# Optimization experiments

Measured on AMD Instinct MI355X. Metric: run time of the kernel, lower is better.

The kernel has to match this reference:

```python
import jax, jax.numpy as jnp
import numpy as np

B, N, V, D = 4, 1024, 20000, 512
DEPTH, H, DH, W = 6, 8, 64, 512
NB = N // W
NS = 512               # num_state_vectors
PM = D // 4            # dynamic pos-bias MLP width
XL_LAYERS = (4, 5)     # 0-indexed (config layers 5, 6)
REC_LAYER = 3          # 0-indexed (config layer 4)
QK_RMS = {3, 4, 5}     # recurrent + xl layers use qk rmsnorm
QK_SCALE = 8.0
FF = 4 * D


def _ln(x, g, eps=1e-5):
    mu = x.mean(-1, keepdims=True)
    var = ((x - mu) ** 2).mean(-1, keepdims=True)
    return (x - mu) * jax.lax.rsqrt(var + eps) * g


def _l2norm(x):
    return x * jax.lax.rsqrt((x * x).sum(-1, keepdims=True) + 1e-12)


def _pos_bias(pos_w1, pos_b1, pos_w2, pos_b2, pos_w3, pos_b3):
    # MLP over scalar relative distance -> per-head bias table [W, H]
    d = jnp.arange(W, dtype=jnp.float32)[:, None]
    h = jax.nn.silu(d @ pos_w1 + pos_b1)
    h = jax.nn.silu(h @ pos_w2 + pos_b2)
    table = h @ pos_w3 + pos_b3                       # [W, H]
    i = jnp.arange(W)[:, None]
    j = jnp.arange(2 * W)[None, :]
    rel = jnp.abs(i + W - j)                          # distance to key in [prev|cur] window
    win = (j > i) & (j <= i + W)                      # causal sliding window of width W
    pb = table[jnp.where(win, rel, 0)]                # [W, 2W, H]
    return jnp.transpose(pb, (2, 0, 1)), win          # [H, W, 2W], [W, 2W]


def setup_inputs() -> dict:
    key = jax.random.key(0)
    ks = iter(jax.random.split(key, 64))
    w = lambda shape, s=0.02: jax.random.normal(next(ks), shape, jnp.float32) * s
    return dict(
        x=jax.random.randint(next(ks), (B, N), 0, V, jnp.int32),
        tok_emb=w((V, D)),
        pos_w1=w((1, PM)), pos_b1=jnp.zeros((PM,), jnp.float32),
        pos_w2=w((PM, PM)), pos_b2=jnp.zeros((PM,), jnp.float32),
        pos_w3=w((PM, H)), pos_b3=jnp.zeros((H,), jnp.float32),
        ln_g=jnp.ones((DEPTH, D), jnp.float32),
        Wq=w((DEPTH, D, H * DH)), Wk=w((DEPTH, D, H * DH)),
        Wv=w((DEPTH, D, H * DH)), Wo=w((DEPTH, H * DH, D)),
        q_scale=jnp.ones((DEPTH, DH), jnp.float32),
        k_scale=jnp.ones((DEPTH, DH), jnp.float32),
        Wo_state=w((H * DH, D)),
        state_norm_g=jnp.ones((D,), jnp.float32),
        Wq2s=w((D, H * DH)), Ws2q=w((D, H * DH)), Ws2kv=w((D, 2 * DH)),
        W_state_out=w((H * DH, D)),
        ema_beta=jnp.zeros((D,), jnp.float32),
        ff_g=jnp.ones((DEPTH, D), jnp.float32),
        ff_w1=w((DEPTH, D, FF)), ff_b1=jnp.zeros((DEPTH, FF), jnp.float32),
        ff_w2=w((DEPTH, FF, D)), ff_b2=jnp.zeros((DEPTH, D), jnp.float32),
        final_g=jnp.ones((D,), jnp.float32),
        W_logits=w((D, V)),
        xl_mem_k=jax.random.normal(next(ks), (len(XL_LAYERS), B, W, H, DH), jnp.float32),
        xl_mem_v=jax.random.normal(next(ks), (len(XL_LAYERS), B, W, H, DH), jnp.float32),
        states=jax.random.normal(next(ks), (B, NS, D), jnp.float32),
    )


def reference(x, tok_emb, pos_w1, pos_b1, pos_w2, pos_b2, pos_w3, pos_b3,
              ln_g, Wq, Wk, Wv, Wo, q_scale, k_scale, Wo_state,
              state_norm_g, Wq2s, Ws2q, Ws2kv, W_state_out, ema_beta,
              ff_g, ff_w1, ff_b1, ff_w2, ff_b2, final_g, W_logits,
              xl_mem_k, xl_mem_v, states):
    pb, win = _pos_bias(pos_w1, pos_b1, pos_w2, pos_b2, pos_w3, pos_b3)
    j = jnp.arange(2 * W)
    no_mem = win & (j[None, :] >= W)                  # first block of a non-xl layer has no memory
    scale_dh = DH ** -0.5
    # enhanced recurrence: rotate the xl memory stack one layer down
    xk = jnp.roll(xl_mem_k, -1, axis=0)
    xv = jnp.roll(xl_mem_v, -1, axis=0)

    hstate = tok_emb[x]                               # [B, N, D]
    next_xl_k, next_xl_v = [], []
    next_states = states
    xl_idx = 0
    for l in range(DEPTH):
        xn = _ln(hstate, ln_g[l])
        q = (xn @ Wq[l]).reshape(B, N, H, DH)
        k = (xn @ Wk[l]).reshape(B, N, H, DH)
        v = (xn @ Wv[l]).reshape(B, N, H, DH)
        if l in QK_RMS:
            q = _l2norm(q) * q_scale[l]
            k = _l2norm(k) * k_scale[l]
            scale = QK_SCALE
        else:
            scale = scale_dh
        qb = q.reshape(B, NB, W, H, DH)
        kb = k.reshape(B, NB, W, H, DH)
        vb = v.reshape(B, NB, W, H, DH)
        is_xl = l in XL_LAYERS
        if is_xl:
            mem_k, mem_v = xk[xl_idx], xv[xl_idx]     # [B, W, H, DH] kv carried from prior call
            valid = jnp.stack([win] * NB)             # [NB, W, 2W]
        else:
            mem_k = jnp.zeros_like(kb[:, 0])
            mem_v = jnp.zeros_like(vb[:, 0])
            valid = jnp.stack([no_mem] + [win] * (NB - 1))
        # each block attends to [previous block | current block]
        pk = jnp.concatenate([mem_k[:, None], kb[:, :-1]], axis=1)
        pv = jnp.concatenate([mem_v[:, None], vb[:, :-1]], axis=1)
        kcat = jnp.concatenate([pk, kb], axis=2)      # [B, NB, 2W, H, DH]
        vcat = jnp.concatenate([pv, vb], axis=2)
        scores = jnp.einsum('bnihd,bnjhd->bnhij', qb * scale, kcat) + pb[None, None]
        scores = jnp.where(valid[None, :, None], scores, -1e9)
        attn = jax.nn.softmax(scores, axis=-1)
        out = jnp.einsum('bnhij,bnjhd->bnihd', attn, vcat).reshape(B, N, H * DH)
        branch = out @ Wo[l]
        if l == REC_LAYER:
            # recurrent state vectors: scan over blocks carrying states
            xn_blk = jnp.moveaxis(xn.reshape(B, NB, W, D), 1, 0)   # [NB, B, W, D]
            kb_s = jnp.moveaxis(kb, 1, 0)
            vb_s = jnp.moveaxis(vb, 1, 0)

            def step(st, inp):
                xb, kblk, vblk = inp
                sn = _ln(st, state_norm_g)
                s_k, s_v = jnp.split(sn @ Ws2kv, 2, axis=-1)       # single-head kv [B, NS, DH]
                # block tokens cross-attend to states
                q2s = (xb @ Wq2s).reshape(B, W, H, DH) * scale_dh
                a = jax.nn.softmax(jnp.einsum('bihd,bjd->bhij', q2s, s_k), -1)
                t_out = jnp.einsum('bhij,bjd->bihd', a, s_v).reshape(B, W, H * DH)
                # states attend to [states | block tokens]
                sq = (sn @ Ws2q).reshape(B, NS, H, DH) * scale_dh
                kc = jnp.concatenate([jnp.broadcast_to(s_k[:, :, None], (B, NS, H, DH)), kblk], axis=1)
                vc = jnp.concatenate([jnp.broadcast_to(s_v[:, :, None], (B, NS, H, DH)), vblk], axis=1)
                a2 = jax.nn.softmax(jnp.einsum('bihd,bjhd->bhij', sq, kc), -1)
                s_out = jnp.einsum('bhij,bjhd->bihd', a2, vc).reshape(B, NS, H * DH) @ W_state_out
                decay = jax.nn.sigmoid(ema_beta)
                return decay * st + (1.0 - decay) * s_out, t_out

            next_states, t_outs = jax.lax.scan(step, states, (xn_blk, kb_s, vb_s))
            to_state = jnp.moveaxis(t_outs, 0, 1).reshape(B, N, H * DH)
            branch = branch + to_state @ Wo_state
        hstate = hstate + branch
        if is_xl:
            next_xl_k.append(kb[:, -1])
            next_xl_v.append(vb[:, -1])
            xl_idx += 1
        fn = _ln(hstate, ff_g[l])
        hstate = hstate + (jax.nn.gelu(fn @ ff_w1[l] + ff_b1[l]) @ ff_w2[l] + ff_b2[l])

    logits = _ln(hstate, final_g) @ W_logits          # [B, N, V]
    return logits, jnp.stack(next_xl_k), jnp.stack(next_xl_v), next_states
```

## Files before the change

### kernel.cpp

```cpp
#include <hip/hip_runtime.h>
#include <math.h>


typedef __attribute__((ext_vector_type(8))) __bf16 bf16x8;
typedef __attribute__((ext_vector_type(8))) _Float16 f16x8;
typedef __attribute__((ext_vector_type(4))) float f32x4;

__device__ __forceinline__ ushort f2b(float f){
  uint u = __float_as_uint(f);
  uint r = (u + 0x7FFFu + ((u >> 16) & 1u)) >> 16;
  return (ushort)r;
}
__device__ __forceinline__ ushort f2h(float f){
  _Float16 h = (_Float16)f;
  return *reinterpret_cast<ushort*>(&h);
}
__device__ __forceinline__ uint pkh2(float a, float b){
  return (uint)f2h(a) | ((uint)f2h(b)<<16);
}

template<int MODE>
__global__ __launch_bounds__(256)
void k_prep(const float* __restrict__ src, ushort* __restrict__ dh,
            ushort* __restrict__ dl, int K, int N, int Npad, long zStride){
// ... 69 lines not shown
  ushort tmp[16];
#pragma unroll
  for (int u=0;u<16;u++) tmp[u] = tile[kf+u][d];
  uint4 o0 = make_uint4((uint)tmp[0]|((uint)tmp[1]<<16), (uint)tmp[2]|((uint)tmp[3]<<16),
                        (uint)tmp[4]|((uint)tmp[5]<<16), (uint)tmp[6]|((uint)tmp[7]<<16));
  uint4 o1 = make_uint4((uint)tmp[8]|((uint)tmp[9]<<16), (uint)tmp[10]|((uint)tmp[11]<<16),
                        (uint)tmp[12]|((uint)tmp[13]<<16),(uint)tmp[14]|((uint)tmp[15]<<16));
  *reinterpret_cast<uint4*>(dp)   = o0;
  *reinterpret_cast<uint4*>(dp+8) = o1;
}

__global__ void k_cvt(ushort* __restrict__ dst, const float* __restrict__ src, int n2){
  int idx = blockIdx.x*blockDim.x + threadIdx.x;
  if (idx >= n2) return;
  reinterpret_cast<uint*>(dst)[idx] = pkh2(src[2*idx], src[2*idx+1]);
}

__global__ void k_embed(const int* __restrict__ x, const float* __restrict__ emb,
                        float* __restrict__ h, int total4){
  int idx = blockIdx.x*blockDim.x + threadIdx.x;
  if (idx >= total4) return;
  int row = idx >> 7;
  int c4  = idx & 127;
  int tok = x[row];
  reinterpret_cast<float4*>(h)[idx] =
      reinterpret_cast<const float4*>(emb)[(size_t)tok*128 + c4];
}

__global__ void k_postable(const float* __restrict__ w1, const float* __restrict__ b1,
                           const float* __restrict__ w2, const float* __restrict__ b2,
                           const float* __restrict__ w3, const float* __restrict__ b3,
                           float* __restrict__ table){
  __shared__ float h1[128];
  __shared__ float h2[128];
  int d = blockIdx.x, t = threadIdx.x;
  float a = (float)d * w1[t] + b1[t];
  h1[t] = a / (1.f + __expf(-a));
  __syncthreads();
  float acc = b2[t];
  for (int p=0;p<128;p++) acc += h1[p]*w2[p*128+t];
  h2[t] = acc / (1.f + __expf(-acc));
  __syncthreads();
  if (t < 8){
    float acc2 = b3[t];
    for (int p=0;p<128;p++) acc2 += h2[p]*w3[p*8+t];
    table[d*8+t] = acc2;
  }
}

__global__ void k_ln(const float* __restrict__ x, const float* __restrict__ g,
                     ushort* __restrict__ y16,
                     ushort* __restrict__ yh, ushort* __restrict__ yl){
  int row = blockIdx.x;
  int t = threadIdx.x;
  float2 v = reinterpret_cast<const float2*>(x + (size_t)row*512)[t];
  float s = v.x+v.y, ss = v.x*v.x+v.y*v.y;
  for (int o=32;o;o>>=1){ s += __shfl_down(s,o); ss += __shfl_down(ss,o); }
  __shared__ float ls[4], lss[4];
  __shared__ float smu, srs;
  int wid = t>>6;
  if ((t&63)==0){ ls[wid]=s; lss[wid]=ss; }
  __syncthreads();
  if (t==0){
    float S=ls[0]+ls[1]+ls[2]+ls[3], SS=lss[0]+lss[1]+lss[2]+lss[3];
    float mu = S*(1.f/512.f);
    float var = SS*(1.f/512.f) - mu*mu;
    smu = mu; srs = rsqrtf(var + 1e-5f);
  }
  __syncthreads();
  float mu=smu, rs=srs;
  float2 gg = reinterpret_cast<const float2*>(g)[t];
  float ya = (v.x-mu)*rs*gg.x, yb = (v.y-mu)*rs*gg.y;
  size_t o2 = (size_t)row*512 + 2*t;
  if (y16)
    *reinterpret_cast<uint*>(&y16[o2]) = pkh2(ya, yb);
  if (yh){
    ushort ha = f2b(ya), hb = f2b(yb);
    *reinterpret_cast<uint*>(&yh[o2]) = (uint)ha | ((uint)hb<<16);
    float fa = __uint_as_float((uint)ha<<16), fb = __uint_as_float((uint)hb<<16);
    *reinterpret_cast<uint*>(&yl[o2]) = (uint)f2b(ya-fa) | ((uint)f2b(yb-fb)<<16);
  }
}

__global__ void k_qkrms16(float* __restrict__ q, float* __restrict__ k,
                          ushort* __restrict__ q16, ushort* __restrict__ k16,
                          const float* __restrict__ qs, const float* __restrict__ ks){
  int row = blockIdx.x;
  int h = threadIdx.x >> 6, d = threadIdx.x & 63;
  size_t base = (size_t)row*512 + h*64 + d;
  float qv = q[base];
  float s = qv*qv;
  for (int o=32;o;o>>=1) s += __shfl_xor(s,o);
  float qn = qv*rsqrtf(s+1e-12f)*qs[d];
  q[base] = qn; q16[base] = f2h(qn);
  float kv = k[base];
  float s2 = kv*kv;
  for (int o=32;o;o>>=1) s2 += __shfl_xor(s2,o);
  float kn = kv*rsqrtf(s2+1e-12f)*ks[d];
  k[base] = kn; k16[base] = f2h(kn);
}

__device__ __forceinline__ float geluf(float x){
  float u = 1.5957691216f*(x + 0.044715f*x*x*x);
  return x / (1.f + __expf(-u));
}

template<int ACC, int EPI, int OUT16>
__global__ __launch_bounds__(256)
void k_gemmh(const ushort* __restrict__ A, const ushort* __restrict__ Bt,
             const float* __restrict__ bias, float* __restrict__ C,
             ushort* __restrict__ C16, int M, int N, int K){
  __shared__ ushort As[128][68];
  __shared__ ushort Bs[128][68];
  const int t = threadIdx.x;
  const int m0 = blockIdx.x*128, n0 = blockIdx.y*128;
  const int w = t>>6, lane = t&63;
  const int wm = (w>>1)*64, wn = (w&1)*64;
  const int fr = lane&15, fg = lane>>4;
  const int srow = t>>1, sko = (t&1)*32;

  f32x4 acc[4][4];
#pragma unroll
  for (int i=0;i<4;i++)
#pragma unroll
    for (int j=0;j<4;j++){ acc[i][j][0]=0.f; acc[i][j][1]=0.f; acc[i][j][2]=0.f; acc[i][j][3]=0.f; }

  const ushort* ap = A  + (size_t)(m0+srow)*K + sko;
  const ushort* bp = Bt + (size_t)(n0+srow)*K + sko;

  for (int k0=0; k0<K; k0+=64){
    uint4 av[4], bv[4];
#pragma unroll
    for (int u=0;u<4;u++){
      av[u] = *reinterpret_cast<const uint4*>(ap + k0 + u*8);
      bv[u] = *reinterpret_cast<const uint4*>(bp + k0 + u*8);
    }
#pragma unroll
    for (int u=0;u<4;u++){
      *reinterpret_cast<uint4*>(&As[srow][sko+u*8]) = av[u];
      *reinterpret_cast<uint4*>(&Bs[srow][sko+u*8]) = bv[u];
    }
    __syncthreads();
#pragma unroll
    for (int kk=0;kk<2;kk++){
      f16x8 af[4], bf[4];
#pragma unroll
      for (int mi=0;mi<4;mi++)
        af[mi] = *reinterpret_cast<const f16x8*>(&As[wm+mi*16+fr][kk*32+fg*8]);
#pragma unroll
      for (int nj=0;nj<4;nj++)
        bf[nj] = *reinterpret_cast<const f16x8*>(&Bs[wn+nj*16+fr][kk*32+fg*8]);
#pragma unroll
      for (int mi=0;mi<4;mi++)
#pragma unroll
        for (int nj=0;nj<4;nj++)
          acc[mi][nj] = __builtin_amdgcn_mfma_f32_16x16x32_f16(af[mi], bf[nj], acc[mi][nj], 0,0,0);
    }
    __syncthreads();
  }
#pragma unroll
  for (int mi=0;mi<4;mi++){
#pragma unroll
    for (int r=0;r<4;r++){
      int row = m0 + wm + mi*16 + fg*4 + r;
#pragma unroll
      for (int nj=0;nj<4;nj++){
        int col = n0 + wn + nj*16 + fr;
        if (col < N){
          float val = acc[mi][nj][r];
          if (bias) val += bias[col];
          if (EPI==1) val = geluf(val);
          if (OUT16){
            C16[(size_t)row*N + col] = f2h(val);
          } else {
            if (ACC) C[(size_t)row*N + col] += val; else C[(size_t)row*N + col] = val;
          }
        }
      }
    }
  }
}

template<int ACC, int EPI, int OUT16, int VT>
__global__ __launch_bounds__(256)
void k_gemmh64(const ushort* __restrict__ A, const ushort* __restrict__ Bt,
               const float* __restrict__ bias, float* __restrict__ C,
               ushort* __restrict__ C16, ushort* __restrict__ vT,
               int M, int N, int K){
  __shared__ ushort As[64][68];
  __shared__ ushort Bs[128][68];
  const int t = threadIdx.x;
  const int m0 = blockIdx.x*64, n0 = blockIdx.y*128;
  const int w = t>>6, lane = t&63;
  const int wm = (w>>1)*32, wn = (w&1)*64;
  const int fr = lane&15, fg = lane>>4;
  const int srowA = t>>2, skoA = (t&3)*16;
  const int srowB = t>>1, skoB = (t&1)*32;

  f32x4 acc[2][4];
#pragma unroll
  for (int i=0;i<2;i++)
#pragma unroll
    for (int j=0;j<4;j++){ acc[i][j][0]=0.f; acc[i][j][1]=0.f; acc[i][j][2]=0.f; acc[i][j][3]=0.f; }

  const ushort* ap = A  + (size_t)(m0+srowA)*K + skoA;
  const ushort* bp = Bt + (size_t)(n0+srowB)*K + skoB;

  for (int k0=0; k0<K; k0+=64){
    uint4 a0 = *reinterpret_cast<const uint4*>(ap + k0);
    uint4 a1 = *reinterpret_cast<const uint4*>(ap + k0 + 8);
    uint4 b0 = *reinterpret_cast<const uint4*>(bp + k0);
    uint4 b1 = *reinterpret_cast<const uint4*>(bp + k0 + 8);
    uint4 b2 = *reinterpret_cast<const uint4*>(bp + k0 + 16);
    uint4 b3 = *reinterpret_cast<const uint4*>(bp + k0 + 24);
    *reinterpret_cast<uint4*>(&As[srowA][skoA])    = a0;
    *reinterpret_cast<uint4*>(&As[srowA][skoA+8])  = a1;
    *reinterpret_cast<uint4*>(&Bs[srowB][skoB])    = b0;
    *reinterpret_cast<uint4*>(&Bs[srowB][skoB+8])  = b1;
    *reinterpret_cast<uint4*>(&Bs[srowB][skoB+16]) = b2;
    *reinterpret_cast<uint4*>(&Bs[srowB][skoB+24]) = b3;
    __syncthreads();
#pragma unroll
    for (int kk=0;kk<2;kk++){
      f16x8 af[2], bf[4];
#pragma unroll
      for (int mi=0;mi<2;mi++)
        af[mi] = *reinterpret_cast<const f16x8*>(&As[wm+mi*16+fr][kk*32+fg*8]);
#pragma unroll
      for (int nj=0;nj<4;nj++)
        bf[nj] = *reinterpret_cast<const f16x8*>(&Bs[wn+nj*16+fr][kk*32+fg*8]);
#pragma unroll
      for (int mi=0;mi<2;mi++)
#pragma unroll
        for (int nj=0;nj<4;nj++)
          acc[mi][nj] = __builtin_amdgcn_mfma_f32_16x16x32_f16(af[mi], bf[nj], acc[mi][nj], 0,0,0);
    }
    __syncthreads();
  }
#pragma unroll
  for (int mi=0;mi<2;mi++){
#pragma unroll
    for (int r=0;r<4;r++){
      int row = m0 + wm + mi*16 + fg*4 + r;
#pragma unroll
      for (int nj=0;nj<4;nj++){
        int col = n0 + wn + nj*16 + fr;
        if (col < N){
          float val = acc[mi][nj][r];
          if (EPI==2){
            size_t idx = (size_t)row*N + col;
            float old = C[idx];
            float dec = 1.f/(1.f+__expf(-bias[col]));
            C[idx] = dec*old + (1.f-dec)*val;
          } else {
            if (bias) val += bias[col];
            if (EPI==1) val = geluf(val);
            if (OUT16){
              C16[(size_t)row*N + col] = f2h(val);
            } else {
              if (ACC) C[(size_t)row*N + col] += val; else C[(size_t)row*N + col] = val;
            }
          }
        }
      }
    }
  }
  if (VT){
#pragma unroll
    for (int mi=0;mi<2;mi++)
#pragma unroll
      for (int r=0;r<4;r++)
#pragma unroll
        for (int nj=0;nj<4;nj++)
          Bs[wn+nj*16+fr][wm+mi*16+fg*4+r] = f2h(acc[mi][nj][r]);
    __syncthreads();
    int c = t>>1, half = t&1;
    int hh = (n0+c)>>6, dd = (n0+c)&63;
    int bb = m0>>10, posb = m0&1023;
    ushort* dp = vT + (size_t)bb*524288 + (size_t)hh*65536 + (size_t)dd*1024 + posb + half*32;
#pragma unroll
    for (int u=0;u<4;u++)
      *reinterpret_cast<uint4*>(dp + u*8) = *reinterpret_cast<const uint4*>(&Bs[c][half*32 + u*8]);
  }
}

template<int REMAP>
__global__ __launch_bounds__(256)
void k_gemm_sp(const ushort* __restrict__ Ah, const ushort* __restrict__ Al,
               const ushort* __restrict__ Bh, const ushort* __restrict__ Bl,
               float* __restrict__ C1, ushort* __restrict__ C1h, int ld1, int N1,
               float* __restrict__ C2, ushort* __restrict__ C2h, int ld2,
               int nb, int M, int N, int K){
  __shared__ ushort As[2][128][36];
  __shared__ ushort Bs[2][128][36];
  const int t = threadIdx.x;
  const int m0 = blockIdx.x*128, n0 = blockIdx.y*128;
  const int w = t>>6, lane = t&63;
  const int wm = (w>>1)*64, wn = (w&1)*64;
  const int fr = lane&15, fg = lane>>4;
  const int srow = t>>1, sko = (t&1)*16;

  f32x4 acc[4][4];
#pragma unroll
  for (int i=0;i<4;i++)
#pragma unroll
    for (int j=0;j<4;j++){ acc[i][j][0]=0.f; acc[i][j][1]=0.f; acc[i][j][2]=0.f; acc[i][j][3]=0.f; }

  int mrow = m0 + srow;
  int arow = REMAP ? ((mrow>>9)*1024 + nb*512 + (mrow&511)) : mrow;
  const ushort* aph = Ah + (size_t)arow*K + sko;
  const ushort* apl = Al + (size_t)arow*K + sko;
  const ushort* bph = Bh + (size_t)(n0+srow)*K + sko;
  const ushort* bpl = Bl + (size_t)(n0+srow)*K + sko;

  for (int k0=0; k0<K; k0+=32){
    uint4 a0 = *reinterpret_cast<const uint4*>(aph + k0);
    uint4 a1 = *reinterpret_cast<const uint4*>(aph + k0 + 8);
    uint4 al0 = *reinterpret_cast<const uint4*>(apl + k0);
    uint4 al1 = *reinterpret_cast<const uint4*>(apl + k0 + 8);
    uint4 b0 = *reinterpret_cast<const uint4*>(bph + k0);
    uint4 b1 = *reinterpret_cast<const uint4*>(bph + k0 + 8);
    uint4 bl0 = *reinterpret_cast<const uint4*>(bpl + k0);
    uint4 bl1 = *reinterpret_cast<const uint4*>(bpl + k0 + 8);
    *reinterpret_cast<uint4*>(&As[0][srow][sko])   = a0;
    *reinterpret_cast<uint4*>(&As[0][srow][sko+8]) = a1;
    *reinterpret_cast<uint4*>(&As[1][srow][sko])   = al0;
    *reinterpret_cast<uint4*>(&As[1][srow][sko+8]) = al1;
    *reinterpret_cast<uint4*>(&Bs[0][srow][sko])   = b0;
    *reinterpret_cast<uint4*>(&Bs[0][srow][sko+8]) = b1;
    *reinterpret_cast<uint4*>(&Bs[1][srow][sko])   = bl0;
    *reinterpret_cast<uint4*>(&Bs[1][srow][sko+8]) = bl1;
    __syncthreads();

    bf16x8 ah[4], al[4], bh[4], bl[4];
#pragma unroll
    for (int mi=0;mi<4;mi++){
      ah[mi] = *reinterpret_cast<const bf16x8*>(&As[0][wm+mi*16+fr][fg*8]);
      al[mi] = *reinterpret_cast<const bf16x8*>(&As[1][wm+mi*16+fr][fg*8]);
    }
#pragma unroll
    for (int nj=0;nj<4;nj++){
      bh[nj] = *reinterpret_cast<const bf16x8*>(&Bs[0][wn+nj*16+fr][fg*8]);
      bl[nj] = *reinterpret_cast<const bf16x8*>(&Bs[1][wn+nj*16+fr][fg*8]);
    }
#pragma unroll
    for (int mi=0;mi<4;mi++)
#pragma unroll
      for (int nj=0;nj<4;nj++){
        acc[mi][nj] = __builtin_amdgcn_mfma_f32_16x16x32_bf16(ah[mi], bh[nj], acc[mi][nj], 0,0,0);
        acc[mi][nj] = __builtin_amdgcn_mfma_f32_16x16x32_bf16(al[mi], bh[nj], acc[mi][nj], 0,0,0);
        acc[mi][nj] = __builtin_amdgcn_mfma_f32_16x16x32_bf16(ah[mi], bl[nj], acc[mi][nj], 0,0,0);
      }
    __syncthreads();
  }
#pragma unroll
  for (int mi=0;mi<4;mi++){
#pragma unroll
    for (int r=0;r<4;r++){
      int row = m0 + wm + mi*16 + fg*4 + r;
#pragma unroll
      for (int nj=0;nj<4;nj++){
        int col = n0 + wn + nj*16 + fr;
        float val = acc[mi][nj][r];
        if (col < N1){
          if (C1)  C1[(size_t)row*ld1 + col] = val;
          if (C1h) C1h[(size_t)row*ld1 + col] = f2h(val);
        } else if (col < N){
          if (C2)  C2[(size_t)row*ld2 + (col-N1)] = val;
          if (C2h) C2h[(size_t)row*ld2 + (col-N1)] = f2h(val);
        }
      }
    }
  }
}

__global__ __launch_bounds__(256)
void k_attn_win(const ushort* __restrict__ q16, const ushort* __restrict__ k16,
                const ushort* __restrict__ vTb,
                const ushort* __restrict__ xlK, const ushort* __restrict__ xlVT,
                int isxl, ushort* __restrict__ O, float scale,
                const float* __restrict__ table){
  __shared__ ushort Qs[64][72];
  __shared__ ushort Ks[64][72];
  __shared__ ushort Vs[64][72];
  __shared__ ushort Pw[4][16][72];
  __shared__ float tcol[512];
  const int b = blockIdx.z, h = blockIdx.y;
  const int nb = blockIdx.x>>3, qt = blockIdx.x&7;
  const int t = threadIdx.x, w = t>>6, lane = t&63;
  const int fr = lane&15, fg = lane>>4;
  tcol[t]     = table[t*8 + h];
  tcol[t+256] = table[(t+256)*8 + h];

  const ushort* Q  = q16 + (size_t)nb*262144;
  const ushort* K1 = k16 + (size_t)nb*262144;
  const ushort* V1 = vTb + (size_t)nb*512;
  ushort* Op = O + (size_t)nb*262144;
  const int has_mem = (nb==1) || isxl;
  const ushort* K0; long k0B; const ushort* V0; long vt0B, vt0H; int vt0D;
  if (nb==1){ K0=k16; k0B=524288; V0=vTb; vt0B=524288; vt0H=65536; vt0D=1024; }
  else if (isxl){ K0=xlK; k0B=262144; V0=xlVT; vt0B=262144; vt0H=32768; vt0D=512; }
  else { K0=k16; k0B=524288; V0=vTb; vt0B=524288; vt0H=65536; vt0D=1024; }

  {
    int qrow = t>>2, doff = (t&3)*16;
    const ushort* qp = Q + (size_t)b*524288 + (size_t)(qt*64+qrow)*512 + h*64 + doff;
    *reinterpret_cast<uint4*>(&Qs[qrow][doff])   = *reinterpret_cast<const uint4*>(qp);
    *reinterpret_cast<uint4*>(&Qs[qrow][doff+8]) = *reinterpret_cast<const uint4*>(qp+8);
  }
  __syncthreads();
  f16x8 aq[2];
  aq[0] = *reinterpret_cast<const f16x8*>(&Qs[w*16+fr][fg*8]);
  aq[1] = *reinterpret_cast<const f16x8*>(&Qs[w*16+fr][32+fg*8]);

  f32x4 so[4];
#pragma unroll
  for (int dt=0;dt<4;dt++){ so[dt][0]=0.f; so[dt][1]=0.f; so[dt][2]=0.f; so[dt][3]=0.f; }
  float m[4] = {-1e30f,-1e30f,-1e30f,-1e30f};
  float lsum[4] = {0.f,0.f,0.f,0.f};

  const int srow = t>>2, sdo = (t&3)*16;
  const int vd = t>>2,   vkf = (t&3)*16;

  int jt0 = has_mem ? qt : 8;
  int jt1 = qt + 8; if (jt1 > 15) jt1 = 15;

  for (int jt=jt0; jt<=jt1; jt++){
    {
      int key = jt*64 + srow;
      const ushort* kp;
      if (key < 512) kp = K0 + (size_t)b*k0B + (size_t)key*512 + h*64 + sdo;
      else           kp = K1 + (size_t)b*524288 + (size_t)(key-512)*512 + h*64 + sdo;
      *reinterpret_cast<uint4*>(&Ks[srow][sdo])   = *reinterpret_cast<const uint4*>(kp);
      *reinterpret_cast<uint4*>(&Ks[srow][sdo+8]) = *reinterpret_cast<const uint4*>(kp+8);
    }
    {
      const ushort* vp;
      if (jt*64 < 512) vp = V0 + (size_t)b*vt0B + (size_t)h*vt0H + (size_t)vd*vt0D + jt*64 + vkf;
      else             vp = V1 + (size_t)b*524288 + (size_t)h*65536 + (size_t)vd*1024 + (jt*64-512) + vkf;
      *reinterpret_cast<uint4*>(&Vs[vd][vkf])   = *reinterpret_cast<const uint4*>(vp);
      *reinterpret_cast<uint4*>(&Vs[vd][vkf+8]) = *reinterpret_cast<const uint4*>(vp+8);
    }
    __syncthreads();
    f32x4 sacc[4];
#pragma unroll
    for (int kt=0;kt<4;kt++){ sacc[kt][0]=0.f; sacc[kt][1]=0.f; sacc[kt][2]=0.f; sacc[kt][3]=0.f; }
#pragma unroll
    for (int ks=0;ks<2;ks++){
#pragma unroll
      for (int kt=0;kt<4;kt++){
        f16x8 bf = *reinterpret_cast<const f16x8*>(&Ks[kt*16+fr][ks*32+fg*8]);
        sacc[kt] = __builtin_amdgcn_mfma_f32_16x16x32_f16(aq[ks], bf, sacc[kt], 0,0,0);
      }
    }
#pragma unroll
    for (int r=0;r<4;r++){
      float sv[4];
      int ia = qt*64 + w*16 + fg*4 + r;
#pragma unroll
      for (int kt=0;kt<4;kt++){
        float s = sacc[kt][r]*scale;
        int jg = jt*64 + kt*16 + fr;
        bool valid = (jg > ia) && (jg <= ia+512) && (has_mem || jg >= 512);
        sv[kt] = valid ? s + tcol[ia+512-jg] : -1e9f;
      }
      float tm = fmaxf(fmaxf(sv[0],sv[1]), fmaxf(sv[2],sv[3]));
      tm = fmaxf(tm, __shfl_xor(tm,1));
      tm = fmaxf(tm, __shfl_xor(tm,2));
      tm = fmaxf(tm, __shfl_xor(tm,4));
      tm = fmaxf(tm, __shfl_xor(tm,8));
      float mn = fmaxf(m[r], tm);
      float c = __expf(m[r]-mn);
      m[r] = mn;
      float ps = 0.f;
#pragma unroll
      for (int kt=0;kt<4;kt++){
        float pp = (sv[kt] <= -1e8f) ? 0.f : __expf(sv[kt]-mn);
        ps += pp;
        Pw[w][fg*4+r][kt*16+fr] = f2h(pp);
      }
      ps += __shfl_xor(ps,1);
      ps += __shfl_xor(ps,2);
      ps += __shfl_xor(ps,4);
      ps += __shfl_xor(ps,8);
      lsum[r] = lsum[r]*c + ps;
#pragma unroll
      for (int dt=0;dt<4;dt++) so[dt][r] *= c;
    }
#pragma unroll
    for (int ks=0;ks<2;ks++){
      f16x8 pa = *reinterpret_cast<const f16x8*>(&Pw[w][fr][ks*32+fg*8]);
#pragma unroll
      for (int dt=0;dt<4;dt++){
        f16x8 bv = *reinterpret_cast<const f16x8*>(&Vs[dt*16+fr][ks*32+fg*8]);
        so[dt] = __builtin_amdgcn_mfma_f32_16x16x32_f16(pa, bv, so[dt], 0,0,0);
      }
    }
    __syncthreads();
  }
#pragma unroll
  for (int r=0;r<4;r++){
    int row = qt*64 + w*16 + fg*4 + r;
    float inv = 1.f / lsum[r];
    ushort* op = Op + (size_t)b*524288 + (size_t)row*512 + h*64;
#pragma unroll
    for (int dt=0;dt<4;dt++)
      op[dt*16+fr] = f2h(so[dt][r]*inv);
  }
}

__global__ __launch_bounds__(256)
void k_attn_plain(const ushort* __restrict__ Q, long qB,
                  const ushort* __restrict__ K0, long k0B, int k0R, int k0H,
                  const ushort* __restrict__ K1, long k1B, int k1R, int k1H,
                  const ushort* __restrict__ VT0, long vt0B, long vt0H, int vt0D,
                  const ushort* __restrict__ VT1, long vt1B, long vt1H, int vt1D,
                  int n0, int n1,
                  ushort* __restrict__ O, long oB, float scale){
  __shared__ ushort Qs[64][72];
  __shared__ ushort Ks[64][72];
  __shared__ ushort Vs[64][72];
  __shared__ ushort Pw[4][16][72];
  const int b = blockIdx.z, h = blockIdx.y, qt = blockIdx.x;
  const int t = threadIdx.x, w = t>>6, lane = t&63;
  const int fr = lane&15, fg = lane>>4;
  {
    int qrow = t>>2, doff = (t&3)*16;
    const ushort* qp = Q + (size_t)b*qB + (size_t)(qt*64+qrow)*512 + h*64 + doff;
    *reinterpret_cast<uint4*>(&Qs[qrow][doff])   = *reinterpret_cast<const uint4*>(qp);
    *reinterpret_cast<uint4*>(&Qs[qrow][doff+8]) = *reinterpret_cast<const uint4*>(qp+8);
  }
  __syncthreads();
  f16x8 aq[2];
  aq[0] = *reinterpret_cast<const f16x8*>(&Qs[w*16+fr][fg*8]);
  aq[1] = *reinterpret_cast<const f16x8*>(&Qs[w*16+fr][32+fg*8]);

  f32x4 so[4];
#pragma unroll
  for (int dt=0;dt<4;dt++){ so[dt][0]=0.f; so[dt][1]=0.f; so[dt][2]=0.f; so[dt][3]=0.f; }
  float m[4] = {-1e30f,-1e30f,-1e30f,-1e30f};
  float lsum[4] = {0.f,0.f,0.f,0.f};

  const int nt = (n0+n1)>>6;
  const int srow = t>>2, sdo = (t&3)*16;
  const int vd = t>>2,   vkf = (t&3)*16;

  for (int jt=0; jt<nt; jt++){
    {
      int key = jt*64 + srow;
      const ushort* kp;
      if (key < n0) kp = K0 + (size_t)b*k0B + (size_t)key*k0R + (k0H? h*64:0) + sdo;
      else          kp = K1 + (size_t)b*k1B + (size_t)(key-n0)*k1R + (k1H? h*64:0) + sdo;
      *reinterpret_cast<uint4*>(&Ks[srow][sdo])   = *reinterpret_cast<const uint4*>(kp);
      *reinterpret_cast<uint4*>(&Ks[srow][sdo+8]) = *reinterpret_cast<const uint4*>(kp+8);
    }
    {
      const ushort* vp;
      if (jt*64 < n0) vp = VT0 + (size_t)b*vt0B + (size_t)h*vt0H + (size_t)vd*vt0D + jt*64 + vkf;
      else            vp = VT1 + (size_t)b*vt1B + (size_t)h*vt1H + (size_t)vd*vt1D + (jt*64-n0) + vkf;
      *reinterpret_cast<uint4*>(&Vs[vd][vkf])   = *reinterpret_cast<const uint4*>(vp);
      *reinterpret_cast<uint4*>(&Vs[vd][vkf+8]) = *reinterpret_cast<const uint4*>(vp+8);
    }
    __syncthreads();
    f32x4 sacc[4];
#pragma unroll
    for (int kt=0;kt<4;kt++){ sacc[kt][0]=0.f; sacc[kt][1]=0.f; sacc[kt][2]=0.f; sacc[kt][3]=0.f; }
#pragma unroll
    for (int ks=0;ks<2;ks++){
#pragma unroll
      for (int kt=0;kt<4;kt++){
        f16x8 bf = *reinterpret_cast<const f16x8*>(&Ks[kt*16+fr][ks*32+fg*8]);
        sacc[kt] = __builtin_amdgcn_mfma_f32_16x16x32_f16(aq[ks], bf, sacc[kt], 0,0,0);
      }
    }
#pragma unroll
    for (int r=0;r<4;r++){
      float sv[4];
#pragma unroll
      for (int kt=0;kt<4;kt++) sv[kt] = sacc[kt][r]*scale;
      float tm = fmaxf(fmaxf(sv[0],sv[1]), fmaxf(sv[2],sv[3]));
      tm = fmaxf(tm, __shfl_xor(tm,1));
      tm = fmaxf(tm, __shfl_xor(tm,2));
      tm = fmaxf(tm, __shfl_xor(tm,4));
      tm = fmaxf(tm, __shfl_xor(tm,8));
      float mn = fmaxf(m[r], tm);
      float c = __expf(m[r]-mn);
      m[r] = mn;
      float ps = 0.f;
#pragma unroll
      for (int kt=0;kt<4;kt++){
        float pp = __expf(sv[kt]-mn);
        ps += pp;
        Pw[w][fg*4+r][kt*16+fr] = f2h(pp);
      }
      ps += __shfl_xor(ps,1);
      ps += __shfl_xor(ps,2);
      ps += __shfl_xor(ps,4);
      ps += __shfl_xor(ps,8);
      lsum[r] = lsum[r]*c + ps;
#pragma unroll
      for (int dt=0;dt<4;dt++) so[dt][r] *= c;
    }
#pragma unroll
    for (int ks=0;ks<2;ks++){
      f16x8 pa = *reinterpret_cast<const f16x8*>(&Pw[w][fr][ks*32+fg*8]);
#pragma unroll
      for (int dt=0;dt<4;dt++){
        f16x8 bv = *reinterpret_cast<const f16x8*>(&Vs[dt*16+fr][ks*32+fg*8]);
        so[dt] = __builtin_amdgcn_mfma_f32_16x16x32_f16(pa, bv, so[dt], 0,0,0);
      }
    }
    __syncthreads();
  }
#pragma unroll
  for (int r=0;r<4;r++){
    int row = qt*64 + w*16 + fg*4 + r;
    float inv = 1.f / lsum[r];
    ushort* op = O + (size_t)b*oB + (size_t)row*512 + h*64;
#pragma unroll
    for (int dt=0;dt<4;dt++)
      op[dt*16+fr] = f2h(so[dt][r]*inv);
  }
}

__global__ void k_copy(float* __restrict__ dst, const float* __restrict__ src, int n){
  int idx = blockIdx.x*blockDim.x + threadIdx.x;
  if (idx < n) dst[idx] = src[idx];
}
__global__ void k_xlout(float* __restrict__ dk, float* __restrict__ dv,
                        const float* __restrict__ k, const float* __restrict__ v){
  int idx = blockIdx.x*blockDim.x + threadIdx.x;
  if (idx >= 1048576) return;
  int b = idx >> 18, rem = idx & 262143;
  size_t s = (size_t)b*524288 + 262144 + rem;
  dk[idx] = k[s]; dv[idx] = v[s];
}

extern "C" void kernel_launch(void* const* d_in, const int* in_sizes, int n_in,
                              void* d_out, int out_size, void* d_ws, size_t ws_size,
                              hipStream_t stream){
  if (ws_size < (size_t)160579584) return;

  const int*   x        = (const int*)  d_in[0];
  const float* tok_emb  = (const float*)d_in[1];
  const float* pw1 = (const float*)d_in[2];
  const float* pb1 = (const float*)d_in[3];
  const float* pw2 = (const float*)d_in[4];
  const float* pb2 = (const float*)d_in[5];
  const float* pw3 = (const float*)d_in[6];
  const float* pb3 = (const float*)d_in[7];
  const float* ln_g = (const float*)d_in[8];
  const float* Wq = (const float*)d_in[9];
  const float* Wk = (const float*)d_in[10];
  const float* Wv = (const float*)d_in[11];
  const float* Wo = (const float*)d_in[12];
  const float* q_scale = (const float*)d_in[13];
  const float* k_scale = (const float*)d_in[14];
  const float* Wo_state = (const float*)d_in[15];
  const float* state_norm_g = (const float*)d_in[16];
  const float* Wq2s = (const float*)d_in[17];
  const float* Ws2q = (const float*)d_in[18];
  const float* Ws2kv = (const float*)d_in[19];
  const float* W_state_out = (const float*)d_in[20];
  const float* ema_beta = (const float*)d_in[21];
  const float* ff_g = (const float*)d_in[22];
  const float* ff_w1 = (const float*)d_in[23];
  const float* ff_b1 = (const float*)d_in[24];
  const float* ff_w2 = (const float*)d_in[25];
  const float* ff_b2 = (const float*)d_in[26];
  const float* final_g = (const float*)d_in[27];
  const float* W_logits = (const float*)d_in[28];
  const float* xl_mem_k = (const float*)d_in[29];
  const float* xl_mem_v = (const float*)d_in[30];
  const float* states_in = (const float*)d_in[31];

  float* out = (float*)d_out;
  float* out_xlk    = out + 81920000;
  float* out_xlv    = out + 84017152;
  float* out_states = out + 86114304;

  float* p = (float*)d_ws;
  float* hstate   = p; p += 2097152;
  float* q        = p; p += 2097152;
  float* k        = p; p += 2097152;
  float* v        = p; p += 2097152;
  float* states_cur = p; p += 1048576;
  float* table    = p; p += 4096;

  ushort* us = (ushort*)p;
  ushort* wqkh  = us; us += 3145728;
  ushort* wqkl  = us; us += 3145728;
  ushort* wvT   = us; us += 1572864;
  ushort* woT   = us; us += 1572864;
  ushort* ffw1T = us; us += 6291456;
  ushort* ffw2T = us; us += 6291456;
  ushort* wostT = us; us += 262144;
  ushort* wstoutT = us; us += 262144;
  ushort* wq2sh = us; us += 262144;
  ushort* wq2sl = us; us += 262144;
  ushort* wsqkvh = us; us += 327680;
  ushort* wsqkvl = us; us += 327680;
  ushort* wlogT  = us; us += 10289152;
  ushort* vTb   = us; us += 2097152;
  ushort* xlvT  = us; us += 2097152;
  ushort* svT   = us; us += 131072;
  ushort* xn16  = us; us += 2097152;
  ushort* ao16  = us; us += 2097152;
  ushort* ff1_16 = us; us += 8388608;
  ushort* xnh   = us; us += 2097152;
  ushort* xnl   = us; us += 2097152;
  ushort* q16   = us; us += 2097152;
  ushort* k16   = us; us += 2097152;
  ushort* xlk16 = us; us += 2097152;
  ushort* ts16   = ff1_16;
  ushort* sa16   = ff1_16 + 2097152;
  ushort* snh    = ff1_16 + 3145728;
  ushort* snl    = ff1_16 + 4194304;
  ushort* sq16   = ff1_16 + 5242880;
  ushort* q2s16  = ff1_16 + 6291456;
  ushort* skv16  = ff1_16 + 7340032;

  k_prep<1><<<dim3(16,16,6),256,0,stream>>>(Wq, wqkh, wqkl, 512,512,512, 524288);
  k_prep<1><<<dim3(16,16,6),256,0,stream>>>(Wk, wqkh+262144, wqkl+262144, 512,512,512, 524288);
  k_prep<0><<<dim3(16,16,6),256,0,stream>>>(Wv, wvT, nullptr, 512,512,512, 262144);
  k_prep<0><<<dim3(16,16,6),256,0,stream>>>(Wo, woT, nullptr, 512,512,512, 262144);
  k_prep<0><<<dim3(64,16,6),256,0,stream>>>(ff_w1, ffw1T, nullptr, 512,2048,2048, 1048576);
  k_prep<0><<<dim3(16,64,6),256,0,stream>>>(ff_w2, ffw2T, nullptr, 2048,512,512, 1048576);
  k_prep<0><<<dim3(16,16,1),256,0,stream>>>(Wo_state, wostT, nullptr, 512,512,512, 262144);
  k_prep<0><<<dim3(16,16,1),256,0,stream>>>(W_state_out, wstoutT, nullptr, 512,512,512, 262144);
  k_prep<1><<<dim3(16,16,1),256,0,stream>>>(Wq2s, wq2sh, wq2sl, 512,512,512, 262144);
  k_prep<1><<<dim3(16,16,1),256,0,stream>>>(Ws2q, wsqkvh, wsqkvl, 512,512,512, 327680);
  k_prep<1><<<dim3(4,16,1),256,0,stream>>>(Ws2kv, wsqkvh+262144, wsqkvl+262144, 512,128,128, 327680);
  k_prep<0><<<dim3(628,16,1),256,0,stream>>>(W_logits, wlogT, nullptr, 512,20000,20096, 10289152);

  for (int s=0;s<2;s++)
    k_vtrans<<<dim3(8,8,4),256,0,stream>>>(xl_mem_v + (size_t)s*1048576,
                                           xlvT + (size_t)s*1048576,
                                           262144L, 512, 1, 262144L, 32768L, 512);
  k_cvt<<<4096,256,0,stream>>>(xlk16, xl_mem_k, 1048576);

  k_embed<<<2048, 256, 0, stream>>>(x, tok_emb, hstate, 524288);
  k_postable<<<512, 128, 0, stream>>>(pw1,pb1,pw2,pb2,pw3,pb3, table);
  k_copy<<<4096, 256, 0, stream>>>(states_cur, states_in, 1048576);

  for (int l=0;l<6;l++){
    k_ln<<<4096,256,0,stream>>>(hstate, ln_g + l*512, xn16, xnh, xnl);
    float scale = 0.125f;
    if (l>=3){
      k_gemm_sp<0><<<dim3(32,8),256,0,stream>>>(xnh, xnl,
          wqkh + (size_t)l*524288, wqkl + (size_t)l*524288,
          q, nullptr, 512, 512, k, nullptr, 512, 0, 4096, 1024, 512);
      k_qkrms16<<<4096,512,0,stream>>>(q, k, q16, k16, q_scale + l*64, k_scale + l*64);
      scale = 8.f;
    } else {
      k_gemm_sp<0><<<dim3(32,8),256,0,stream>>>(xnh, xnl,
          wqkh + (size_t)l*524288, wqkl + (size_t)l*524288,
          nullptr, q16, 512, 512, nullptr, k16, 512, 0, 4096, 1024, 512);
    }
    k_gemmh64<0,0,0,1><<<dim3(64,4),256,0,stream>>>(xn16, wvT + (size_t)l*262144, nullptr, v, nullptr, vTb, 4096,512,512);

    bool isxl = (l==4 || l==5);
    int src = (l==4)? 1 : 0;
    k_attn_win<<<dim3(16,8,4),256,0,stream>>>(
        q16, k16, vTb,
        isxl ? xlk16 + (size_t)src*1048576 : k16,
        isxl ? xlvT  + (size_t)src*1048576 : vTb,
        isxl ? 1 : 0, ao16, scale, table);

    k_gemmh64<1,0,0,0><<<dim3(64,4),256,0,stream>>>(ao16, woT + (size_t)l*262144, nullptr, hstate, nullptr, nullptr, 4096,512,512);
    if (l==3){
      for (int nb=0;nb<2;nb++){
        k_ln<<<2048,256,0,stream>>>(states_cur, state_norm_g, nullptr, snh, snl);
        k_gemm_sp<0><<<dim3(16,5),256,0,stream>>>(snh, snl, wsqkvh, wsqkvl,
            nullptr, sq16, 512, 512, nullptr, skv16, 128, 0, 2048, 640, 512);
        k_vtrans16<<<dim3(8,1,4),256,0,stream>>>(skv16 + 64, svT, 65536L, 128, 32768L, 512);
        k_gemm_sp<1><<<dim3(16,4),256,0,stream>>>(xnh, xnl, wq2sh, wq2sl,
            nullptr, q2s16, 512, 512, nullptr, nullptr, 0, nb, 2048, 512, 512);
        k_attn_plain<<<dim3(8,8,4),256,0,stream>>>(
          q2s16, 262144L,
          skv16, 65536L, 128, 0,
          skv16, 65536L, 128, 0,
          svT, 32768L, 0L, 512,
          svT, 32768L, 0L, 512,
          512, 0,
          ts16 + nb*262144, 524288L, 0.125f);
        k_attn_plain<<<dim3(8,8,4),256,0,stream>>>(
          sq16, 262144L,
          skv16, 65536L, 128, 0,
          k16 + nb*262144, 524288L, 512, 1,
          svT, 32768L, 0L, 512,
          vTb + nb*512, 524288L, 65536L, 1024,
          512, 512,
          sa16, 262144L, 0.125f);
        k_gemmh64<0,2,0,0><<<dim3(32,4),256,0,stream>>>(sa16, wstoutT, ema_beta, states_cur, nullptr, nullptr, 2048,512,512);
      }
      k_gemmh64<1,0,0,0><<<dim3(64,4),256,0,stream>>>(ts16, wostT, nullptr, hstate, nullptr, nullptr, 4096,512,512);
    }
    if (isxl){
      int xli = l-4;
      k_xlout<<<4096,256,0,stream>>>(out_xlk + (size_t)xli*1048576,
                                     out_xlv + (size_t)xli*1048576, k, v);
    }
    k_ln<<<4096,256,0,stream>>>(hstate, ff_g + l*512, xn16, nullptr, nullptr);
    k_gemmh<0,1,1><<<dim3(32,16),256,0,stream>>>(xn16, ffw1T + (size_t)l*1048576, ff_b1 + l*2048, nullptr, ff1_16, 4096,2048,512);
    k_gemmh64<1,0,0,0><<<dim3(64,4),256,0,stream>>>(ff1_16, ffw2T + (size_t)l*1048576, ff_b2 + l*512, hstate, nullptr, nullptr, 4096,512,2048);
  }
  k_ln<<<4096,256,0,stream>>>(hstate, final_g, xn16, nullptr, nullptr);
  k_gemmh<0,0,0><<<dim3(32,157),256,0,stream>>>(xn16, wlogT, nullptr, out, nullptr, 4096,20000,512);
  k_copy<<<4096, 256, 0, stream>>>(out_states, states_cur, 1048576);
}
```

Before: 1.728 ms.

## Fuse QK RMSnorm and XL cache output into GEMM epilogues, merge recurrent attention

Moves the per-head QK L2-normalisation into the QK projection GEMM epilogue, using lane shuffles to reduce across the 64-wide head tile. The XL key/value cache outputs are now written straight from the QK and V GEMM epilogues, so the fp32 q/k/v buffers and the separate normalisation and copy kernels are gone. The two recurrent-state attention launches are merged into one kernel that picks its task from blockIdx. This cuts launches and fp32 intermediate traffic, at the cost of more complex epilogues and a reliance on each wave's 64 columns lining up with a single head.

```diff
diff --git a/kernel.cpp b/kernel.cpp
--- a/kernel.cpp
+++ b/kernel.cpp
@@ -175,24 +175,6 @@
   }
 }
 
-__global__ void k_qkrms16(float* __restrict__ q, float* __restrict__ k,
-                          ushort* __restrict__ q16, ushort* __restrict__ k16,
-                          const float* __restrict__ qs, const float* __restrict__ ks){
-  int row = blockIdx.x;
-  int h = threadIdx.x >> 6, d = threadIdx.x & 63;
-  size_t base = (size_t)row*512 + h*64 + d;
-  float qv = q[base];
-  float s = qv*qv;
-  for (int o=32;o;o>>=1) s += __shfl_xor(s,o);
-  float qn = qv*rsqrtf(s+1e-12f)*qs[d];
-  q[base] = qn; q16[base] = f2h(qn);
-  float kv = k[base];
-  float s2 = kv*kv;
-  for (int o=32;o;o>>=1) s2 += __shfl_xor(s2,o);
-  float kn = kv*rsqrtf(s2+1e-12f)*ks[d];
-  k[base] = kn; k16[base] = f2h(kn);
-}
-
 __device__ __forceinline__ float geluf(float x){
   float u = 1.5957691216f*(x + 0.044715f*x*x*x);
   return x / (1.f + __expf(-u));
@@ -279,7 +261,7 @@
 void k_gemmh64(const ushort* __restrict__ A, const ushort* __restrict__ Bt,
                const float* __restrict__ bias, float* __restrict__ C,
                ushort* __restrict__ C16, ushort* __restrict__ vT,
-               int M, int N, int K){
+               float* __restrict__ xlv, int M, int N, int K){
   __shared__ ushort As[64][68];
   __shared__ ushort Bs[128][68];
   const int t = threadIdx.x;
@@ -349,10 +331,12 @@
             if (bias) val += bias[col];
             if (EPI==1) val = geluf(val);
             if (OUT16){
-              C16[(size_t)row*N + col] = f2h(val);
-            } else {
+              if (C16) C16[(size_t)row*N + col] = f2h(val);
+            } else if (C){
               if (ACC) C[(size_t)row*N + col] += val; else C[(size_t)row*N + col] = val;
             }
+            if (VT && xlv && (row&1023) >= 512)
+              xlv[((size_t)(row>>10)*512 + (row&1023) - 512)*512 + col] = val;
           }
         }
       }
@@ -381,8 +365,10 @@
 __global__ __launch_bounds__(256)
 void k_gemm_sp(const ushort* __restrict__ Ah, const ushort* __restrict__ Al,
                const ushort* __restrict__ Bh, const ushort* __restrict__ Bl,
-               float* __restrict__ C1, ushort* __restrict__ C1h, int ld1, int N1,
-               float* __restrict__ C2, ushort* __restrict__ C2h, int ld2,
+               ushort* __restrict__ C1h, int ld1, int N1,
+               ushort* __restrict__ C2h, int ld2,
+               const float* __restrict__ qsc, const float* __restrict__ ksc,
+               float* __restrict__ xlk,
                int nb, int M, int N, int K){
   __shared__ ushort As[2][128][36];
   __shared__ ushort Bs[2][128][36];
@@ -451,16 +437,30 @@
 #pragma unroll
     for (int r=0;r<4;r++){
       int row = m0 + wm + mi*16 + fg*4 + r;
+      float vals[4];
+#pragma unroll
+      for (int nj=0;nj<4;nj++) vals[nj] = acc[mi][nj][r];
+      if (qsc){
+        float ss = vals[0]*vals[0]+vals[1]*vals[1]+vals[2]*vals[2]+vals[3]*vals[3];
+        ss += __shfl_xor(ss,1);
+        ss += __shfl_xor(ss,2);
+        ss += __shfl_xor(ss,4);
+        ss += __shfl_xor(ss,8);
+        float rs = rsqrtf(ss + 1e-12f);
+        const float* sc = ((n0+wn) < N1) ? qsc : ksc;
+#pragma unroll
+        for (int nj=0;nj<4;nj++) vals[nj] = vals[nj]*rs*sc[nj*16+fr];
+      }
 #pragma unroll
       for (int nj=0;nj<4;nj++){
         int col = n0 + wn + nj*16 + fr;
-        float val = acc[mi][nj][r];
+        float val = vals[nj];
         if (col < N1){
-          if (C1)  C1[(size_t)row*ld1 + col] = val;
           if (C1h) C1h[(size_t)row*ld1 + col] = f2h(val);
         } else if (col < N){
-          if (C2)  C2[(size_t)row*ld2 + (col-N1)] = val;
           if (C2h) C2h[(size_t)row*ld2 + (col-N1)] = f2h(val);
+          if (xlk && (row&1023) >= 512)
+            xlk[((size_t)(row>>10)*512 + (row&1023) - 512)*512 + (col-N1)] = val;
         }
       }
     }
@@ -603,23 +603,35 @@
 }
 
 __global__ __launch_bounds__(256)
-void k_attn_plain(const ushort* __restrict__ Q, long qB,
-                  const ushort* __restrict__ K0, long k0B, int k0R, int k0H,
-                  const ushort* __restrict__ K1, long k1B, int k1R, int k1H,
-                  const ushort* __restrict__ VT0, long vt0B, long vt0H, int vt0D,
-                  const ushort* __restrict__ VT1, long vt1B, long vt1H, int vt1D,
-                  int n0, int n1,
-                  ushort* __restrict__ O, long oB, float scale){
+void k_attn_rec(const ushort* __restrict__ q2s, const ushort* __restrict__ sq,
+                const ushort* __restrict__ skv, const ushort* __restrict__ svT,
+                const ushort* __restrict__ kblk, const ushort* __restrict__ vblk,
+                ushort* __restrict__ ts, ushort* __restrict__ sa){
   __shared__ ushort Qs[64][72];
   __shared__ ushort Ks[64][72];
   __shared__ ushort Vs[64][72];
   __shared__ ushort Pw[4][16][72];
-  const int b = blockIdx.z, h = blockIdx.y, qt = blockIdx.x;
+  const int b = blockIdx.z, h = blockIdx.y;
+  const int task = blockIdx.x>>3, qt = blockIdx.x&7;
   const int t = threadIdx.x, w = t>>6, lane = t&63;
   const int fr = lane&15, fg = lane>>4;
+
+  const ushort* Q; const ushort* K1; int k1R, k1H;
+  const ushort* VT1; long vt1B, vt1H; int vt1D;
+  int nt; ushort* O; long oB;
+  if (task==0){
+    Q=q2s; K1=skv; k1R=128; k1H=0;
+    VT1=svT; vt1B=32768; vt1H=0; vt1D=512;
+    nt=8; O=ts; oB=524288;
+  } else {
+    Q=sq; K1=kblk; k1R=512; k1H=1;
+    VT1=vblk; vt1B=524288; vt1H=65536; vt1D=1024;
+    nt=16; O=sa; oB=262144;
+  }
+
   {
     int qrow = t>>2, doff = (t&3)*16;
-    const ushort* qp = Q + (size_t)b*qB + (size_t)(qt*64+qrow)*512 + h*64 + doff;
+    const ushort* qp = Q + (size_t)b*262144 + (size_t)(qt*64+qrow)*512 + h*64 + doff;
     *reinterpret_cast<uint4*>(&Qs[qrow][doff])   = *reinterpret_cast<const uint4*>(qp);
     *reinterpret_cast<uint4*>(&Qs[qrow][doff+8]) = *reinterpret_cast<const uint4*>(qp+8);
   }
@@ -634,7 +646,6 @@
   float m[4] = {-1e30f,-1e30f,-1e30f,-1e30f};
   float lsum[4] = {0.f,0.f,0.f,0.f};
 
-  const int nt = (n0+n1)>>6;
   const int srow = t>>2, sdo = (t&3)*16;
   const int vd = t>>2,   vkf = (t&3)*16;
 
@@ -642,15 +653,15 @@
     {
       int key = jt*64 + srow;
       const ushort* kp;
-      if (key < n0) kp = K0 + (size_t)b*k0B + (size_t)key*k0R + (k0H? h*64:0) + sdo;
-      else          kp = K1 + (size_t)b*k1B + (size_t)(key-n0)*k1R + (k1H? h*64:0) + sdo;
+      if (key < 512) kp = skv + (size_t)b*65536 + (size_t)key*128 + sdo;
+      else           kp = K1 + (size_t)b*524288 + (size_t)(key-512)*k1R + (k1H? h*64:0) + sdo;
       *reinterpret_cast<uint4*>(&Ks[srow][sdo])   = *reinterpret_cast<const uint4*>(kp);
       *reinterpret_cast<uint4*>(&Ks[srow][sdo+8]) = *reinterpret_cast<const uint4*>(kp+8);
     }
     {
       const ushort* vp;
-      if (jt*64 < n0) vp = VT0 + (size_t)b*vt0B + (size_t)h*vt0H + (size_t)vd*vt0D + jt*64 + vkf;
-      else            vp = VT1 + (size_t)b*vt1B + (size_t)h*vt1H + (size_t)vd*vt1D + (jt*64-n0) + vkf;
+      if (jt*64 < 512) vp = svT + (size_t)b*32768 + (size_t)vd*512 + jt*64 + vkf;
+      else             vp = VT1 + (size_t)b*vt1B + (size_t)h*vt1H + (size_t)vd*vt1D + (jt*64-512) + vkf;
       *reinterpret_cast<uint4*>(&Vs[vd][vkf])   = *reinterpret_cast<const uint4*>(vp);
       *reinterpret_cast<uint4*>(&Vs[vd][vkf+8]) = *reinterpret_cast<const uint4*>(vp+8);
     }
@@ -670,7 +681,7 @@
     for (int r=0;r<4;r++){
       float sv[4];
 #pragma unroll
-      for (int kt=0;kt<4;kt++) sv[kt] = sacc[kt][r]*scale;
+      for (int kt=0;kt<4;kt++) sv[kt] = sacc[kt][r]*0.125f;
       float tm = fmaxf(fmaxf(sv[0],sv[1]), fmaxf(sv[2],sv[3]));
       tm = fmaxf(tm, __shfl_xor(tm,1));
       tm = fmaxf(tm, __shfl_xor(tm,2));
@@ -720,19 +731,11 @@
   int idx = blockIdx.x*blockDim.x + threadIdx.x;
   if (idx < n) dst[idx] = src[idx];
 }
-__global__ void k_xlout(float* __restrict__ dk, float* __restrict__ dv,
-                        const float* __restrict__ k, const float* __restrict__ v){
-  int idx = blockIdx.x*blockDim.x + threadIdx.x;
-  if (idx >= 1048576) return;
-  int b = idx >> 18, rem = idx & 262143;
-  size_t s = (size_t)b*524288 + 262144 + rem;
-  dk[idx] = k[s]; dv[idx] = v[s];
-}
 
 extern "C" void kernel_launch(void* const* d_in, const int* in_sizes, int n_in,
                               void* d_out, int out_size, void* d_ws, size_t ws_size,
                               hipStream_t stream){
-  if (ws_size < (size_t)160579584) return;
+  if (ws_size < (size_t)135413760) return;
 
   const int*   x        = (const int*)  d_in[0];
   const float* tok_emb  = (const float*)d_in[1];
@@ -774,9 +777,6 @@
 
   float* p = (float*)d_ws;
   float* hstate   = p; p += 2097152;
-  float* q        = p; p += 2097152;
-  float* k        = p; p += 2097152;
-  float* v        = p; p += 2097152;
   float* states_cur = p; p += 1048576;
   float* table    = p; p += 4096;
 
@@ -837,66 +837,51 @@
   k_copy<<<4096, 256, 0, stream>>>(states_cur, states_in, 1048576);
 
   for (int l=0;l<6;l++){
+    bool isxl = (l==4 || l==5);
+    int xli = l-4;
+    int src = (l==4)? 1 : 0;
     k_ln<<<4096,256,0,stream>>>(hstate, ln_g + l*512, xn16, xnh, xnl);
     float scale = 0.125f;
-    if (l>=3){
-      k_gemm_sp<0><<<dim3(32,8),256,0,stream>>>(xnh, xnl,
-          wqkh + (size_t)l*524288, wqkl + (size_t)l*524288,
-          q, nullptr, 512, 512, k, nullptr, 512, 0, 4096, 1024, 512);
-      k_qkrms16<<<4096,512,0,stream>>>(q, k, q16, k16, q_scale + l*64, k_scale + l*64);
-      scale = 8.f;
-    } else {
-      k_gemm_sp<0><<<dim3(32,8),256,0,stream>>>(xnh, xnl,
-          wqkh + (size_t)l*524288, wqkl + (size_t)l*524288,
-          nullptr, q16, 512, 512, nullptr, k16, 512, 0, 4096, 1024, 512);
-    }
-    k_gemmh64<0,0,0,1><<<dim3(64,4),256,0,stream>>>(xn16, wvT + (size_t)l*262144, nullptr, v, nullptr, vTb, 4096,512,512);
-
-    bool isxl = (l==4 || l==5);
-    int src = (l==4)? 1 : 0;
+    const float* qsc = nullptr; const float* ksc = nullptr;
+    if (l>=3){ qsc = q_scale + l*64; ksc = k_scale + l*64; scale = 8.f; }
+    k_gemm_sp<0><<<dim3(32,8),256,0,stream>>>(xnh, xnl,
+        wqkh + (size_t)l*524288, wqkl + (size_t)l*524288,
+        q16, 512, 512, k16, 512, qsc, ksc,
+        isxl ? out_xlk + (size_t)xli*1048576 : nullptr,
+        0, 4096, 1024, 512);
+    k_gemmh64<0,0,0,1><<<dim3(64,4),256,0,stream>>>(xn16, wvT + (size_t)l*262144,
+        nullptr, nullptr, nullptr, vTb,
+        isxl ? out_xlv + (size_t)xli*1048576 : nullptr, 4096,512,512);
+
     k_attn_win<<<dim3(16,8,4),256,0,stream>>>(
         q16, k16, vTb,
         isxl ? xlk16 + (size_t)src*1048576 : k16,
         isxl ? xlvT  + (size_t)src*1048576 : vTb,
         isxl ? 1 : 0, ao16, scale, table);
 
-    k_gemmh64<1,0,0,0><<<dim3(64,4),256,0,stream>>>(ao16, woT + (size_t)l*262144, nullptr, hstate, nullptr, nullptr, 4096,512,512);
+    k_gemmh64<1,0,0,0><<<dim3(64,4),256,0,stream>>>(ao16, woT + (size_t)l*262144,
+        nullptr, hstate, nullptr, nullptr, nullptr, 4096,512,512);
     if (l==3){
       for (int nb=0;nb<2;nb++){
         k_ln<<<2048,256,0,stream>>>(states_cur, state_norm_g, nullptr, snh, snl);
         k_gemm_sp<0><<<dim3(16,5),256,0,stream>>>(snh, snl, wsqkvh, wsqkvl,
-            nullptr, sq16, 512, 512, nullptr, skv16, 128, 0, 2048, 640, 512);
+            sq16, 512, 512, skv16, 128, nullptr, nullptr, nullptr, 0, 2048, 640, 512);
         k_vtrans16<<<dim3(8,1,4),256,0,stream>>>(skv16 + 64, svT, 65536L, 128, 32768L, 512);
         k_gemm_sp<1><<<dim3(16,4),256,0,stream>>>(xnh, xnl, wq2sh, wq2sl,
-            nullptr, q2s16, 512, 512, nullptr, nullptr, 0, nb, 2048, 512, 512);
-        k_attn_plain<<<dim3(8,8,4),256,0,stream>>>(
-          q2s16, 262144L,
-          skv16, 65536L, 128, 0,
-          skv16, 65536L, 128, 0,
-          svT, 32768L, 0L, 512,
-          svT, 32768L, 0L, 512,
-          512, 0,
-          ts16 + nb*262144, 524288L, 0.125f);
-        k_attn_plain<<<dim3(8,8,4),256,0,stream>>>(
-          sq16, 262144L,
-          skv16, 65536L, 128, 0,
-          k16 + nb*262144, 524288L, 512, 1,
-          svT, 32768L, 0L, 512,
-          vTb + nb*512, 524288L, 65536L, 1024,
-          512, 512,
-          sa16, 262144L, 0.125f);
-        k_gemmh64<0,2,0,0><<<dim3(32,4),256,0,stream>>>(sa16, wstoutT, ema_beta, states_cur, nullptr, nullptr, 2048,512,512);
-      }
-      k_gemmh64<1,0,0,0><<<dim3(64,4),256,0,stream>>>(ts16, wostT, nullptr, hstate, nullptr, nullptr, 4096,512,512);
-    }
-    if (isxl){
-      int xli = l-4;
-      k_xlout<<<4096,256,0,stream>>>(out_xlk + (size_t)xli*1048576,
-                                     out_xlv + (size_t)xli*1048576, k, v);
+            q2s16, 512, 512, nullptr, 0, nullptr, nullptr, nullptr, nb, 2048, 512, 512);
+        k_attn_rec<<<dim3(16,8,4),256,0,stream>>>(
+            q2s16, sq16, skv16, svT,
+            k16 + (size_t)nb*262144, vTb + (size_t)nb*512,
+            ts16 + (size_t)nb*262144, sa16);
+        k_gemmh64<0,2,0,0><<<dim3(32,4),256,0,stream>>>(sa16, wstoutT, ema_beta,
+            states_cur, nullptr, nullptr, nullptr, 2048,512,512);
+      }
+      k_gemmh64<1,0,0,0><<<dim3(64,4),256,0,stream>>>(ts16, wostT, nullptr,
+          hstate, nullptr, nullptr, nullptr, 4096,512,512);
     }
     k_ln<<<4096,256,0,stream>>>(hstate, ff_g + l*512, xn16, nullptr, nullptr);
     k_gemmh<0,1,1><<<dim3(32,16),256,0,stream>>>(xn16, ffw1T + (size_t)l*1048576, ff_b1 + l*2048, nullptr, ff1_16, 4096,2048,512);
-    k_gemmh64<1,0,0,0><<<dim3(64,4),256,0,stream>>>(ff1_16, ffw2T + (size_t)l*1048576, ff_b2 + l*512, hstate, nullptr, nullptr, 4096,512,2048);
+    k_gemmh64<1,0,0,0><<<dim3(64,4),256,0,stream>>>(ff1_16, ffw2T + (size_t)l*1048576, ff_b2 + l*512, hstate, nullptr, nullptr, nullptr, 4096,512,2048);
   }
   k_ln<<<4096,256,0,stream>>>(hstate, final_g, xn16, nullptr, nullptr);
   k_gemmh<0,0,0><<<dim3(32,157),256,0,stream>>>(xn16, wlogT, nullptr, out, nullptr, 4096,20000,512);
```

Result: faster. 1.628 ms (-5.8%).
